# Performance work log

Hardware: AMD Instinct MI355X
Metric: run time of the kernel (lower is better)

The kernel has to match this reference:

```python
import jax, jax.numpy as jnp
import numpy as np

BIT_SHIFT = 8
H, W = 480, 640
N = 100000
C_IN, C_HID, C_OUT = 96, 576, 96


def setup_inputs() -> dict:
    key = jax.random.key(0)
    ks = jax.random.split(key, 12)
    # --- sparse 2D coordinates (unique active sites on an H x W grid) ---
    rng = np.random.default_rng(0)
    lin = rng.choice(H * W, size=N, replace=False)
    ys, xs = lin // W, lin % W
    grid = -np.ones((H, W), dtype=np.int32)
    grid[ys, xs] = np.arange(N, dtype=np.int32)
    # neighbor index for each of the 9 kernel offsets; -1 where no active neighbor
    nbr = np.empty((9, N), dtype=np.int32)
    k = 0
    for dy in (-1, 0, 1):
        for dx in (-1, 0, 1):
            yn, xn = ys + dy, xs + dx
            valid = (yn >= 0) & (yn < H) & (xn >= 0) & (xn < W)
            idx = grid[np.clip(yn, 0, H - 1), np.clip(xn, 0, W - 1)]
            nbr[k] = np.where(valid, idx, -1)
            k += 1
    # --- int8-valued float features / weights (quantized integer inference) ---
    feats = jnp.round(jnp.clip(30.0 * jax.random.normal(ks[0], (N, C_IN)), -127, 127))
    w1 = jnp.round(jnp.clip(40.0 * jax.random.normal(ks[1], (C_IN, C_HID)), -127, 127))
    b1 = jnp.round(1000.0 * jax.random.normal(ks[2], (C_HID,)))
    w2 = jnp.round(jnp.clip(40.0 * jax.random.normal(ks[3], (9, C_HID)), -127, 127))
    b2 = jnp.round(1000.0 * jax.random.normal(ks[4], (C_HID,)))
    w3 = jnp.round(jnp.clip(40.0 * jax.random.normal(ks[5], (C_HID, C_OUT)), -127, 127))
    b3 = jnp.round(1000.0 * jax.random.normal(ks[6], (C_OUT,)))
    # per-output-channel requantization scaling factors (>= ~1 so round() is nonzero)
    s1 = 1.0 + 3.0 * jax.random.uniform(ks[7], (C_HID,))
    s2 = 1.0 + 3.0 * jax.random.uniform(ks[8], (C_HID,))
    s3 = 1.0 + 3.0 * jax.random.uniform(ks[9], (C_OUT,))
    s_main = 1.0 + 2.0 * jax.random.uniform(ks[10], ())
    s_res = 1.0 + 2.0 * jax.random.uniform(ks[11], ())
    return {"feats": feats, "neighbor_idx": jnp.asarray(nbr), "w1": w1, "b1": b1,
            "w2": w2, "b2": b2, "w3": w3, "b3": b3,
            "s1": s1, "s2": s2, "s3": s3, "s_main": s_main, "s_res": s_res}


def _requant(acc, s):
    # fused integer rescale: multiplier m = round(s) * 2^bit_shift, then /2^(2*bit_shift)
    B = 2.0 ** BIT_SHIFT
    return acc * (jnp.round(s) * B) / (B * B)


def _clamp(x):
    lim = 2.0 ** (BIT_SHIFT - 1)
    return jnp.clip(x, -lim, lim)


def _relu6(x):
    return jnp.clip(x, 0.0, 6.0)


def reference(feats, neighbor_idx, w1, b1, w2, b2, w3, b3, s1, s2, s3, s_main, s_res):
    B = 2.0 ** BIT_SHIFT
    # 1x1 expand conv (dense GEMM over active sites)
    x = _relu6(_clamp(_requant(feats @ w1 + b1, s1)))  # [N, C_HID]
    # depthwise 3x3 sparse conv: gather 9 neighbor taps, mask missing sites
    mask = (neighbor_idx >= 0).astype(x.dtype)               # [9, N]
    gathered = x[jnp.clip(neighbor_idx, 0, None)] * mask[:, :, None]  # [9, N, C_HID]
    dw = jnp.einsum('knc,kc->nc', gathered, w2) + b2
    x = _relu6(_clamp(_requant(dw, s2)))
    # 1x1 project conv
    x = _clamp(_requant(x @ w3 + b3, s3))                    # [N, C_OUT]
    # scaled residual add
    out = jnp.round(s_main) * B * x + jnp.round(s_res) * B * feats
    return out
```

## Files before the change

kernel.cpp:

```cpp
#include <hip/hip_runtime.h>
#include <hip/hip_bf16.h>
#include <hip/hip_fp16.h>

#define NS   100000
#define CIN  96
#define CHID 576
#define COUT 96
#define SPB  16
#define LDH  (CHID + 8)
#define ESPB 32
#define ELDH (CHID + 8)
#define OFFMASK 0x7FFFFFF

typedef float    floatx4 __attribute__((ext_vector_type(4)));
typedef int      intx4   __attribute__((ext_vector_type(4)));
typedef short    short8  __attribute__((ext_vector_type(8)));
typedef _Float16 half8   __attribute__((ext_vector_type(8)));
typedef _Float16 half4   __attribute__((ext_vector_type(4)));

__global__ void prep_kernel(const float* __restrict__ w1, const float* __restrict__ w3,
                            const float* __restrict__ w2,
                            unsigned short* __restrict__ w1T, _Float16* __restrict__ w3T,
                            _Float16* __restrict__ w2h, _Float16* __restrict__ x1h) {
  int i = blockIdx.x * blockDim.x + threadIdx.x;
  if (i >= CHID * CIN) return;
  if (i < CHID) x1h[(size_t)NS * CHID + i] = (_Float16)0.0f;
  if (i < 9 * CHID) w2h[i] = (_Float16)w2[i];
  {
    int h = i / CIN, k = i % CIN;
    w1T[i] = (unsigned short)(__float_as_uint(w1[k * CHID + h]) >> 16);
  }
  {
    int o = i / CHID, k = i % CHID;
    w3T[i] = (_Float16)w3[k * COUT + o];
  }
}

__global__ __launch_bounds__(256) void expand_kernel(
    const float* __restrict__ feats, const float* __restrict__ b1,
    const float* __restrict__ s1, const unsigned short* __restrict__ w1T,
    _Float16* __restrict__ x1h) {
  __shared__ _Float16 xt[ESPB * ELDH];
  const int t = threadIdx.x;
  const int lane = t & 63, wv = t >> 6;
  const int m = lane & 15, quad = lane >> 4;
  const int s0 = blockIdx.x * ESPB;

  short8 bfrag[2][3];
#pragma unroll
  for (int u = 0; u < 2; ++u) {
    const int site = s0 + u * 16 + m;
    const float* frow = feats + (size_t)site * CIN + quad * 8;
#pragma unroll
    for (int kc = 0; kc < 3; ++kc) {
      const float4 lo = *reinterpret_cast<const float4*>(frow + kc * 32);
      const float4 hi = *reinterpret_cast<const float4*>(frow + kc * 32 + 4);
      const float v[8] = {lo.x, lo.y, lo.z, lo.w, hi.x, hi.y, hi.z, hi.w};
#pragma unroll
      for (int j = 0; j < 8; ++j)
        bfrag[u][kc][j] = (short)(__float_as_uint(v[j]) >> 16);
    }
  }

  const int hq = quad * 4;
#pragma unroll 2
  for (int hi = 0; hi < 9; ++hi) {
    const int ht = wv * 9 + hi;
    const unsigned short* wrow = w1T + (ht * 16 + m) * CIN + quad * 8;
    short8 a[3];
#pragma unroll
    for (int kc = 0; kc < 3; ++kc)
      a[kc] = *reinterpret_cast<const short8*>(wrow + kc * 32);

    floatx4 acc[2] = {{0.f, 0.f, 0.f, 0.f}, {0.f, 0.f, 0.f, 0.f}};
#pragma unroll
    for (int kc = 0; kc < 3; ++kc)
#pragma unroll
      for (int u = 0; u < 2; ++u)
        acc[u] = __builtin_amdgcn_mfma_f32_16x16x32_bf16(a[kc], bfrag[u][kc], acc[u], 0, 0, 0);

    const floatx4 bv = *reinterpret_cast<const floatx4*>(b1 + ht * 16 + hq);
    const floatx4 sv = *reinterpret_cast<const floatx4*>(s1 + ht * 16 + hq);
    floatx4 sc;
#pragma unroll
    for (int j = 0; j < 4; ++j) sc[j] = rintf(sv[j]) * (1.0f / 256.0f);

#pragma unroll
    for (int u = 0; u < 2; ++u) {
      half4 r;
#pragma unroll
      for (int j = 0; j < 4; ++j) {
        float v = (acc[u][j] + bv[j]) * sc[j];
        r[j] = (_Float16)fminf(fmaxf(v, 0.0f), 6.0f);
      }
      *reinterpret_cast<half4*>(xt + (u * 16 + m) * ELDH + ht * 16 + hq) = r;
    }
  }
  __syncthreads();

  for (int j = t; j < ESPB * (CHID / 8); j += 256) {
    const int row = j / (CHID / 8), col = j - row * (CHID / 8);
    *reinterpret_cast<half8*>(x1h + (size_t)(s0 + row) * CHID + col * 8) =
        *reinterpret_cast<const half8*>(xt + row * ELDH + col * 8);
  }
}

__global__ __launch_bounds__(256) void dwproj_kernel(
    const int* __restrict__ nbr, const _Float16* __restrict__ w2h,
    const float* __restrict__ b2, const float* __restrict__ s2,
    const _Float16* __restrict__ x1h, const _Float16* __restrict__ w3T,
    const float* __restrict__ feats, const float* __restrict__ b3,
    const float* __restrict__ s3, const float* __restrict__ s_main,
    const float* __restrict__ s_res, float* __restrict__ out) {
  __shared__ _Float16 x2t[SPB * LDH];
  __shared__ _Float16 w2s[9 * CHID];
  __shared__ int offt[SPB * 12];
  __shared__ int scnt[SPB];
  const int t = threadIdx.x;
  const int s0 = blockIdx.x * SPB;

  if (t < SPB) scnt[t] = 0;
  for (int j = t; j < 9 * CHID / 8; j += 256)
    *reinterpret_cast<half8*>(w2s + j * 8) =
        *reinterpret_cast<const half8*>(w2h + j * 8);
  __syncthreads();
  if (t < SPB * 9) {
    const int k = t >> 4, n = t & 15;
    const int idx = nbr[k * NS + s0 + n];
    if (idx >= 0) {
      const int p = atomicAdd(&scnt[n], 1);
      offt[n * 12 + p] = idx * CHID + (k << 27);
    }
  }
  __syncthreads();

#pragma unroll 1
  for (int i = 0; i < 5; ++i) {
    const int w = i * 256 + t;
    if (w < SPB * 72) {
      const int n = w / 72, g = w - n * 72;
      const int c0 = g * 8;
      const int cnt = scnt[n];
      const int* op = offt + n * 12;
      half8 v[9];
      int kk[9];
#pragma unroll
      for (int j = 0; j < 9; ++j)
        if (j < cnt) {
          const int pk = op[j];
          kk[j] = pk >> 27;
          v[j] = *reinterpret_cast<const half8*>(x1h + (size_t)(pk & OFFMASK) + c0);
        }
      float acc[8], scv[8];
      {
        const floatx4 ba = *reinterpret_cast<const floatx4*>(b2 + c0);
        const floatx4 bb = *reinterpret_cast<const floatx4*>(b2 + c0 + 4);
        const floatx4 sa = *reinterpret_cast<const floatx4*>(s2 + c0);
        const floatx4 sb = *reinterpret_cast<const floatx4*>(s2 + c0 + 4);
#pragma unroll
        for (int j = 0; j < 4; ++j) {
          acc[j] = ba[j];  acc[j + 4] = bb[j];
          scv[j] = rintf(sa[j]) * (1.0f / 256.0f);
          scv[j + 4] = rintf(sb[j]) * (1.0f / 256.0f);
        }
      }
#pragma unroll
      for (int j = 0; j < 9; ++j)
        if (j < cnt) {
          const half8 wv = *reinterpret_cast<const half8*>(w2s + kk[j] * CHID + c0);
#pragma unroll
          for (int q = 0; q < 8; ++q)
            acc[q] += (float)v[j][q] * (float)wv[q];
        }
      half8 r;
#pragma unroll
      for (int j = 0; j < 8; ++j) {
        float vv = acc[j] * scv[j];
        r[j] = (_Float16)fminf(fmaxf(vv, 0.0f), 6.0f);
      }
      *reinterpret_cast<half8*>(x2t + n * LDH + c0) = r;
    }
  }
  __syncthreads();

  const int wave = t >> 6, lane = t & 63;
  const int m = lane & 15, quad = lane >> 4;
  const float rsm = rintf(s_main[0]) * 256.0f;
  const float rsr = rintf(s_res[0]) * 256.0f;

  for (int tile = wave; tile < (SPB / 16) * (COUT / 16); tile += 4) {
    const int tm = tile / (COUT / 16);
    const int ot = tile % (COUT / 16);
    floatx4 acc = {0.f, 0.f, 0.f, 0.f};
    const _Float16* arow = w3T + (ot * 16 + m) * CHID + quad * 8;
    const _Float16* blds = x2t + (tm * 16 + m) * LDH + quad * 8;
#pragma unroll
    for (int kc = 0; kc < 18; ++kc) {
      const half8 a = *reinterpret_cast<const half8*>(arow + kc * 32);
      const half8 b = *reinterpret_cast<const half8*>(blds + kc * 32);
      acc = __builtin_amdgcn_mfma_f32_16x16x32_f16(a, b, acc, 0, 0, 0);
    }
    const int site = s0 + tm * 16 + m;
    if (site < NS) {
      const int o0 = ot * 16 + quad * 4;
      const floatx4 b3v = *reinterpret_cast<const floatx4*>(b3 + o0);
      const floatx4 s3v = *reinterpret_cast<const floatx4*>(s3 + o0);
      const floatx4 fv =
          *reinterpret_cast<const floatx4*>(feats + (size_t)site * COUT + o0);
      floatx4 r;
#pragma unroll
      for (int j = 0; j < 4; ++j) {
        float v = (acc[j] + b3v[j]) * (rintf(s3v[j]) * (1.0f / 256.0f));
        v = fminf(fmaxf(v, -128.0f), 128.0f);
        r[j] = rsm * v + rsr * fv[j];
      }
      *reinterpret_cast<floatx4*>(out + (size_t)site * COUT + o0) = r;
    }
  }
}

extern "C" void kernel_launch(void* const* d_in, const int* in_sizes, int n_in,
                              void* d_out, int out_size, void* d_ws, size_t ws_size,
                              hipStream_t stream) {
  const float* feats  = (const float*)d_in[0];
  const int*   nbr    = (const int*)d_in[1];
  const float* w1     = (const float*)d_in[2];
  const float* b1     = (const float*)d_in[3];
  const float* w2     = (const float*)d_in[4];
  const float* b2     = (const float*)d_in[5];
  const float* w3     = (const float*)d_in[6];
  const float* b3     = (const float*)d_in[7];
  const float* s1     = (const float*)d_in[8];
  const float* s2     = (const float*)d_in[9];
  const float* s3     = (const float*)d_in[10];
  const float* s_main = (const float*)d_in[11];
  const float* s_res  = (const float*)d_in[12];
  float* out = (float*)d_out;

  char* ws = (char*)d_ws;
  _Float16*       x1h = (_Float16*)ws;
  unsigned short* w1T = (unsigned short*)(ws + 115201152);
  _Float16*       w3T = (_Float16*)(ws + 115311744);
  _Float16*       w2h = (_Float16*)(ws + 115422336);

  prep_kernel<<<(CHID * CIN + 255) / 256, 256, 0, stream>>>(w1, w3, w2, w1T, w3T, w2h, x1h);
  expand_kernel<<<NS / ESPB, 256, 0, stream>>>(feats, b1, s1, w1T, x1h);
  const int nblk = (NS + SPB - 1) / SPB;
  dwproj_kernel<<<nblk, 256, 0, stream>>>(nbr, w2h, b2, s2, x1h, w3T,
                                          feats, b3, s3, s_main, s_res, out);
}
```

Before: 292.3 us.

## Fuse prep, expand and depthwise-project kernels into one cooperative persistent kernel

Replaces three separate kernel launches with one cooperative kernel on a fixed grid of 625 blocks. Grid-wide syncs separate the weight-prep, expand-GEMM and depthwise+project phases, and each block loops persistently over site chunks. The intent is to remove launch gaps and tail effects between the kernels, and to load the depthwise weights into shared memory once per block rather than once per chunk. The costs are two grid barriers, plus occupancy limited by the cooperative residency requirement and a fixed grid that may underfill or imbalance the GPU. The old three-kernel path is kept as a fallback if the cooperative launch fails.

```diff
diff --git a/kernel.cpp b/kernel.cpp
--- a/kernel.cpp
+++ b/kernel.cpp
@@ -1,6 +1,9 @@
 #include <hip/hip_runtime.h>
+#include <hip/hip_cooperative_groups.h>
 #include <hip/hip_bf16.h>
 #include <hip/hip_fp16.h>
+
+namespace cg = cooperative_groups;
 
 #define NS   100000
 #define CIN  96
@@ -11,12 +14,209 @@
 #define ESPB 32
 #define ELDH (CHID + 8)
 #define OFFMASK 0x7FFFFFF
+#define CGRID 625
 
 typedef float    floatx4 __attribute__((ext_vector_type(4)));
 typedef int      intx4   __attribute__((ext_vector_type(4)));
 typedef short    short8  __attribute__((ext_vector_type(8)));
 typedef _Float16 half8   __attribute__((ext_vector_type(8)));
 typedef _Float16 half4   __attribute__((ext_vector_type(4)));
+
+__global__ __launch_bounds__(256, 3) void fused_kernel(
+    const float* __restrict__ feats, const int* __restrict__ nbr,
+    const float* __restrict__ w1, const float* __restrict__ b1,
+    const float* __restrict__ w2, const float* __restrict__ b2,
+    const float* __restrict__ w3, const float* __restrict__ b3,
+    const float* __restrict__ s1, const float* __restrict__ s2,
+    const float* __restrict__ s3, const float* __restrict__ s_main,
+    const float* __restrict__ s_res, float* __restrict__ out,
+    _Float16* __restrict__ x1h, unsigned short* __restrict__ w1T,
+    _Float16* __restrict__ w3T, _Float16* __restrict__ w2h) {
+  alignas(16) __shared__ char SMEM[ESPB * ELDH * 2];
+  const int t = threadIdx.x, bid = blockIdx.x;
+  cg::grid_group grid = cg::this_grid();
+
+  {
+    const int i = bid * 256 + t;
+    if (i < CHID * CIN) {
+      if (i < CHID) x1h[(size_t)NS * CHID + i] = (_Float16)0.0f;
+      if (i < 9 * CHID) w2h[i] = (_Float16)w2[i];
+      { int h = i / CIN, k = i % CIN;
+        w1T[i] = (unsigned short)(__float_as_uint(w1[k * CHID + h]) >> 16); }
+      { int o = i / CHID, k = i % CHID;
+        w3T[i] = (_Float16)w3[k * COUT + o]; }
+    }
+  }
+  grid.sync();
+
+  {
+    _Float16* xt = (_Float16*)SMEM;
+    const int lane = t & 63, wv = t >> 6;
+    const int m = lane & 15, quad = lane >> 4;
+    for (int c = bid; c < NS / ESPB; c += CGRID) {
+      const int s0 = c * ESPB;
+      short8 bfrag[2][3];
+#pragma unroll
+      for (int u = 0; u < 2; ++u) {
+        const int site = s0 + u * 16 + m;
+        const float* frow = feats + (size_t)site * CIN + quad * 8;
+#pragma unroll
+        for (int kc = 0; kc < 3; ++kc) {
+          const float4 lo = *reinterpret_cast<const float4*>(frow + kc * 32);
+          const float4 hi = *reinterpret_cast<const float4*>(frow + kc * 32 + 4);
+          const float v[8] = {lo.x, lo.y, lo.z, lo.w, hi.x, hi.y, hi.z, hi.w};
+#pragma unroll
+          for (int j = 0; j < 8; ++j)
+            bfrag[u][kc][j] = (short)(__float_as_uint(v[j]) >> 16);
+        }
+      }
+      const int hq = quad * 4;
+#pragma unroll 2
+      for (int hi = 0; hi < 9; ++hi) {
+        const int ht = wv * 9 + hi;
+        const unsigned short* wrow = w1T + (ht * 16 + m) * CIN + quad * 8;
+        short8 a[3];
+#pragma unroll
+        for (int kc = 0; kc < 3; ++kc)
+          a[kc] = *reinterpret_cast<const short8*>(wrow + kc * 32);
+        floatx4 acc[2] = {{0.f, 0.f, 0.f, 0.f}, {0.f, 0.f, 0.f, 0.f}};
+#pragma unroll
+        for (int kc = 0; kc < 3; ++kc)
+#pragma unroll
+          for (int u = 0; u < 2; ++u)
+            acc[u] = __builtin_amdgcn_mfma_f32_16x16x32_bf16(a[kc], bfrag[u][kc], acc[u], 0, 0, 0);
+        const floatx4 bv = *reinterpret_cast<const floatx4*>(b1 + ht * 16 + hq);
+        const floatx4 sv = *reinterpret_cast<const floatx4*>(s1 + ht * 16 + hq);
+        floatx4 sc;
+#pragma unroll
+        for (int j = 0; j < 4; ++j) sc[j] = rintf(sv[j]) * (1.0f / 256.0f);
+#pragma unroll
+        for (int u = 0; u < 2; ++u) {
+          half4 r;
+#pragma unroll
+          for (int j = 0; j < 4; ++j) {
+            float v = (acc[u][j] + bv[j]) * sc[j];
+            r[j] = (_Float16)fminf(fmaxf(v, 0.0f), 6.0f);
+          }
+          *reinterpret_cast<half4*>(xt + (u * 16 + m) * ELDH + ht * 16 + hq) = r;
+        }
+      }
+      __syncthreads();
+      for (int j = t; j < ESPB * (CHID / 8); j += 256) {
+        const int row = j / (CHID / 8), col = j - row * (CHID / 8);
+        *reinterpret_cast<half8*>(x1h + (size_t)(s0 + row) * CHID + col * 8) =
+            *reinterpret_cast<const half8*>(xt + row * ELDH + col * 8);
+      }
+      __syncthreads();
+    }
+  }
+  grid.sync();
+
+  {
+    _Float16* x2t = (_Float16*)SMEM;
+    _Float16* w2s = (_Float16*)(SMEM + 18688);
+    int* offt = (int*)(SMEM + 29056);
+    int* scnt = (int*)(SMEM + 29824);
+    for (int j = t; j < 9 * CHID / 8; j += 256)
+      *reinterpret_cast<half8*>(w2s + j * 8) =
+          *reinterpret_cast<const half8*>(w2h + j * 8);
+    const int wave = t >> 6, lane = t & 63;
+    const int m = lane & 15, quad = lane >> 4;
+    const float rsm = rintf(s_main[0]) * 256.0f;
+    const float rsr = rintf(s_res[0]) * 256.0f;
+
+    for (int c = bid; c < NS / SPB; c += CGRID) {
+      const int s0 = c * SPB;
+      if (t < SPB) scnt[t] = 0;
+      __syncthreads();
+      if (t < SPB * 9) {
+        const int k = t >> 4, n = t & 15;
+        const int idx = nbr[k * NS + s0 + n];
+        if (idx >= 0) {
+          const int p = atomicAdd(&scnt[n], 1);
+          offt[n * 12 + p] = idx * CHID + (k << 27);
+        }
+      }
+      __syncthreads();
+#pragma unroll 1
+      for (int i = 0; i < 5; ++i) {
+        const int w = i * 256 + t;
+        if (w < SPB * 72) {
+          const int n = w / 72, g = w - n * 72;
+          const int c0 = g * 8;
+          const int cnt = scnt[n];
+          const int* op = offt + n * 12;
+          half8 v[9];
+          int kk[9];
+#pragma unroll
+          for (int j = 0; j < 9; ++j)
+            if (j < cnt) {
+              const int pk = op[j];
+              kk[j] = pk >> 27;
+              v[j] = *reinterpret_cast<const half8*>(x1h + (size_t)(pk & OFFMASK) + c0);
+            }
+          float acc[8], scv[8];
+          {
+            const floatx4 ba = *reinterpret_cast<const floatx4*>(b2 + c0);
+            const floatx4 bb = *reinterpret_cast<const floatx4*>(b2 + c0 + 4);
+            const floatx4 sa = *reinterpret_cast<const floatx4*>(s2 + c0);
+            const floatx4 sb = *reinterpret_cast<const floatx4*>(s2 + c0 + 4);
+#pragma unroll
+            for (int j = 0; j < 4; ++j) {
+              acc[j] = ba[j];  acc[j + 4] = bb[j];
+              scv[j] = rintf(sa[j]) * (1.0f / 256.0f);
+              scv[j + 4] = rintf(sb[j]) * (1.0f / 256.0f);
+            }
+          }
+#pragma unroll
+          for (int j = 0; j < 9; ++j)
+            if (j < cnt) {
+              const half8 wv = *reinterpret_cast<const half8*>(w2s + kk[j] * CHID + c0);
+#pragma unroll
+              for (int q = 0; q < 8; ++q)
+                acc[q] += (float)v[j][q] * (float)wv[q];
+            }
+          half8 r;
+#pragma unroll
+          for (int j = 0; j < 8; ++j) {
+            float vv = acc[j] * scv[j];
+            r[j] = (_Float16)fminf(fmaxf(vv, 0.0f), 6.0f);
+          }
+          *reinterpret_cast<half8*>(x2t + n * LDH + c0) = r;
+        }
+      }
+      __syncthreads();
+      for (int tile = wave; tile < (SPB / 16) * (COUT / 16); tile += 4) {
+        const int tm = tile / (COUT / 16);
+        const int ot = tile % (COUT / 16);
+        floatx4 acc = {0.f, 0.f, 0.f, 0.f};
+        const _Float16* arow = w3T + (ot * 16 + m) * CHID + quad * 8;
+        const _Float16* blds = x2t + (tm * 16 + m) * LDH + quad * 8;
+#pragma unroll
+        for (int kc = 0; kc < 18; ++kc) {
+          const half8 a = *reinterpret_cast<const half8*>(arow + kc * 32);
+          const half8 b = *reinterpret_cast<const half8*>(blds + kc * 32);
+          acc = __builtin_amdgcn_mfma_f32_16x16x32_f16(a, b, acc, 0, 0, 0);
+        }
+        const int site = s0 + tm * 16 + m;
+        const int o0 = ot * 16 + quad * 4;
+        const floatx4 b3v = *reinterpret_cast<const floatx4*>(b3 + o0);
+        const floatx4 s3v = *reinterpret_cast<const floatx4*>(s3 + o0);
+        const floatx4 fv =
+            *reinterpret_cast<const floatx4*>(feats + (size_t)site * COUT + o0);
+        floatx4 r;
+#pragma unroll
+        for (int j = 0; j < 4; ++j) {
+          float v = (acc[j] + b3v[j]) * (rintf(s3v[j]) * (1.0f / 256.0f));
+          v = fminf(fmaxf(v, -128.0f), 128.0f);
+          r[j] = rsm * v + rsr * fv[j];
+        }
+        *reinterpret_cast<floatx4*>(out + (size_t)site * COUT + o0) = r;
+      }
+      __syncthreads();
+    }
+  }
+}
 
 __global__ void prep_kernel(const float* __restrict__ w1, const float* __restrict__ w3,
                             const float* __restrict__ w2,
@@ -61,7 +261,6 @@
         bfrag[u][kc][j] = (short)(__float_as_uint(v[j]) >> 16);
     }
   }
-
   const int hq = quad * 4;
 #pragma unroll 2
   for (int hi = 0; hi < 9; ++hi) {
@@ -71,20 +270,17 @@
 #pragma unroll
     for (int kc = 0; kc < 3; ++kc)
       a[kc] = *reinterpret_cast<const short8*>(wrow + kc * 32);
-
     floatx4 acc[2] = {{0.f, 0.f, 0.f, 0.f}, {0.f, 0.f, 0.f, 0.f}};
 #pragma unroll
     for (int kc = 0; kc < 3; ++kc)
 #pragma unroll
       for (int u = 0; u < 2; ++u)
         acc[u] = __builtin_amdgcn_mfma_f32_16x16x32_bf16(a[kc], bfrag[u][kc], acc[u], 0, 0, 0);
-
     const floatx4 bv = *reinterpret_cast<const floatx4*>(b1 + ht * 16 + hq);
     const floatx4 sv = *reinterpret_cast<const floatx4*>(s1 + ht * 16 + hq);
     floatx4 sc;
 #pragma unroll
     for (int j = 0; j < 4; ++j) sc[j] = rintf(sv[j]) * (1.0f / 256.0f);
-
 #pragma unroll
     for (int u = 0; u < 2; ++u) {
       half4 r;
@@ -97,7 +293,6 @@
     }
   }
   __syncthreads();
-
   for (int j = t; j < ESPB * (CHID / 8); j += 256) {
     const int row = j / (CHID / 8), col = j - row * (CHID / 8);
     *reinterpret_cast<half8*>(x1h + (size_t)(s0 + row) * CHID + col * 8) =
@@ -187,7 +382,6 @@
   const int m = lane & 15, quad = lane >> 4;
   const float rsm = rintf(s_main[0]) * 256.0f;
   const float rsr = rintf(s_res[0]) * 256.0f;
-
   for (int tile = wave; tile < (SPB / 16) * (COUT / 16); tile += 4) {
     const int tm = tile / (COUT / 16);
     const int ot = tile % (COUT / 16);
@@ -243,9 +437,17 @@
   _Float16*       w3T = (_Float16*)(ws + 115311744);
   _Float16*       w2h = (_Float16*)(ws + 115422336);
 
-  prep_kernel<<<(CHID * CIN + 255) / 256, 256, 0, stream>>>(w1, w3, w2, w1T, w3T, w2h, x1h);
-  expand_kernel<<<NS / ESPB, 256, 0, stream>>>(feats, b1, s1, w1T, x1h);
-  const int nblk = (NS + SPB - 1) / SPB;
-  dwproj_kernel<<<nblk, 256, 0, stream>>>(nbr, w2h, b2, s2, x1h, w3T,
-                                          feats, b3, s3, s_main, s_res, out);
+  void* args[] = {(void*)&feats, (void*)&nbr, (void*)&w1, (void*)&b1,
+                  (void*)&w2, (void*)&b2, (void*)&w3, (void*)&b3,
+                  (void*)&s1, (void*)&s2, (void*)&s3, (void*)&s_main,
+                  (void*)&s_res, (void*)&out, (void*)&x1h, (void*)&w1T,
+                  (void*)&w3T, (void*)&w2h};
+  hipError_t err = hipLaunchCooperativeKernel((const void*)fused_kernel,
+                                              dim3(CGRID), dim3(256), args, 0, stream);
+  if (err != hipSuccess) {
+    prep_kernel<<<(CHID * CIN + 255) / 256, 256, 0, stream>>>(w1, w3, w2, w1T, w3T, w2h, x1h);
+    expand_kernel<<<NS / ESPB, 256, 0, stream>>>(feats, b1, s1, w1T, x1h);
+    dwproj_kernel<<<NS / SPB, 256, 0, stream>>>(nbr, w2h, b2, s2, x1h, w3T,
+                                                feats, b3, s3, s_main, s_res, out);
+  }
 }
```

After: 506.9 us. 1.73x slower.
